# Optimization experiments

Hardware: AMD Instinct MI355X
Metric: run time of the kernel (lower is better)

## Reference

```python
import jax, jax.numpy as jnp
import numpy as np

B, C, H, W = 8, 512, 64, 128
K = 19          # num_classes
BH, BW = 2, 4   # bin_size
N = BH * BW     # bin_num
CI = C // 2     # feat_inner


def setup_inputs() -> dict:
    ks = jax.random.split(jax.random.key(0), 10)
    def nrm(k, shape, s=0.02):
        return jax.random.normal(k, shape, jnp.float32) * s
    return {
        "x": jax.random.normal(ks[0], (B, C, H, W), jnp.float32),
        "conv_cam_w": nrm(ks[1], (K, C)),
        "conv_cam_b": jnp.zeros((K,), jnp.float32),
        "gcn_w1": nrm(ks[2], (N, N), 0.1),
        "gcn_a": jnp.full((N,), 0.25, jnp.float32),
        "gcn_w2": nrm(ks[3], (C, C)),
        "fuse_w": nrm(ks[4], (1, N), 0.1),
        "fuse_b": jnp.zeros((1,), jnp.float32),
        "relu_a": jnp.full((1,), 0.25, jnp.float32),
        "q_w": nrm(ks[5], (CI, C)),
        "q_b": jnp.zeros((CI,), jnp.float32),
        "k_w": nrm(ks[6], (CI, C)),
        "k_b": jnp.zeros((CI,), jnp.float32),
        "v_w": nrm(ks[7], (CI, C)),
        "v_b": jnp.zeros((CI,), jnp.float32),
        "out_w": nrm(ks[8], (C, CI)),
        "bn_gamma": jnp.ones((C,), jnp.float32),
        "bn_beta": jnp.zeros((C,), jnp.float32),
        "out_a": jnp.full((C,), 0.25, jnp.float32),
    }


def _prelu(x, a):
    return jnp.maximum(x, 0) + a * jnp.minimum(x, 0)


def _split(t):
    # [b, cc, H, W] -> [b, N, rh*rw, cc]  (patch_split)
    b, cc = t.shape[0], t.shape[1]
    rh, rw = H // BH, W // BW
    t = t.reshape(b, cc, BH, rh, BW, rw).transpose(0, 2, 4, 3, 5, 1)
    return t.reshape(b, N, rh * rw, cc)


def _caam(x, conv_cam_w, conv_cam_b, gcn_w1, gcn_a, gcn_w2, fuse_w, fuse_b,
          relu_a, q_w, q_b, k_w, k_b, v_w, v_b, out_w, bn_gamma, bn_beta, out_a):
    b = x.shape[0]
    rh, rw = H // BH, W // BW
    # CAM (1x1 conv) + adaptive avg pool to bins + sigmoid
    cam = jnp.einsum('bchw,kc->bkhw', x, conv_cam_w) + conv_cam_b[None, :, None, None]
    cls_score = jax.nn.sigmoid(cam.reshape(b, K, BH, rh, BW, rw).mean((3, 5)))  # [b,K,BH,BW]
    cam_p = _split(cam)   # [b,N,P,K]
    x_p = _split(x)       # [b,N,P,C]
    bin_conf = cls_score.reshape(b, K, N).transpose(0, 2, 1)[..., None]  # [b,N,K,1]
    pix_conf = jax.nn.softmax(cam_p, axis=2)
    local = jnp.einsum('bnpk,bnpc->bnkc', pix_conf, x_p) * bin_conf  # [b,N,K,C]
    # GCN: conv1 over bin dim, PReLU(residual), Linear over channels
    t = jnp.einsum('nm,bmkc->bnkc', gcn_w1, local)
    t = _prelu(t + local, gcn_a[None, :, None, None])
    local = jnp.einsum('bnkc,dc->bnkd', t, gcn_w2)
    # fuse bins -> single global descriptor, PReLU(1)
    glob = jnp.einsum('on,bnkc->bokc', fuse_w, local) + fuse_b[None, :, None, None]  # [b,1,K,C]
    glob = _prelu(glob[:, 0], relu_a[0])  # [b,K,C]
    # QKV attention over bins (key/value over K class slots)
    q = jnp.einsum('bnpc,ic->bnpi', x_p, q_w) + q_b       # [b,N,P,CI]
    key = jnp.einsum('bnkc,ic->bnki', local, k_w) + k_b   # [b,N,K,CI]
    val = jnp.einsum('bkc,ic->bki', glob, v_w) + v_b      # [b,K,CI] (shared across bins)
    aff = jax.nn.softmax(jnp.einsum('bnpi,bnki->bnpk', q, key), axis=-1)
    out = jnp.einsum('bnpk,bki->bnpi', aff, val)          # [b,N,P,CI]
    # patch_recover -> [b,CI,H,W]
    out = out.reshape(b, BH, BW, rh, rw, CI).transpose(0, 5, 1, 3, 2, 4).reshape(b, CI, H, W)
    # conv_out: 1x1 conv (no bias) + BatchNorm2d (batch stats) + PReLU(C)
    y = jnp.einsum('bihw,ci->bchw', out, out_w)
    mu = y.mean((0, 2, 3), keepdims=True)
    var = y.var((0, 2, 3), keepdims=True)
    y = (y - mu) * jax.lax.rsqrt(var + 1e-5)
    y = y * bn_gamma[None, :, None, None] + bn_beta[None, :, None, None]
    y = _prelu(y, out_a[None, :, None, None])
    return x + y


def reference(x, conv_cam_w, conv_cam_b, gcn_w1, gcn_a, gcn_w2, fuse_w, fuse_b,
              relu_a, q_w, q_b, k_w, k_b, v_w, v_b, out_w, bn_gamma, bn_beta, out_a):
    return _caam(x, conv_cam_w, conv_cam_b, gcn_w1, gcn_a, gcn_w2, fuse_w, fuse_b,
                 relu_a, q_w, q_b, k_w, k_b, v_w, v_b, out_w, bn_gamma, bn_beta, out_a)
```

## Files before the change

### kernel.cpp

```cpp
#include <hip/hip_runtime.h>
#include <cstdint>
#include <cstddef>

#define B_ 8
#define C_ 512
#define H_ 64
#define W_ 128
#define HW_ 8192
#define K_ 19
#define N_ 8
#define P_ 1024
#define CI_ 256

typedef unsigned short u16;
typedef unsigned int u32;
typedef __attribute__((ext_vector_type(8))) short bf16x8;
typedef __attribute__((ext_vector_type(4))) float f32x4;

__device__ __forceinline__ u16 f2bf(float f) {
  u32 u = __float_as_uint(f);
  u32 r = (u + 0x7FFFu + ((u >> 16) & 1u)) >> 16;
  return (u16)r;
}
__device__ __forceinline__ float bf2f(u16 h) {
  return __uint_as_float(((u32)h) << 16);
}

__device__ __forceinline__ float blockSum256(float v, float* red4) {
#pragma unroll
  for (int o = 32; o > 0; o >>= 1) v += __shfl_down(v, o, 64);
  __syncthreads();
  if ((threadIdx.x & 63) == 0) red4[threadIdx.x >> 6] = v;
  __syncthreads();
  return red4[0] + red4[1] + red4[2] + red4[3];
}

__device__ __forceinline__ float blockMax256(float v, float* red4) {
#pragma unroll
  for (int o = 32; o > 0; o >>= 1) v = fmaxf(v, __shfl_down(v, o, 64));
  __syncthreads();
  if ((threadIdx.x & 63) == 0) red4[threadIdx.x >> 6] = v;
  __syncthreads();
  return fmaxf(fmaxf(red4[0], red4[1]), fmaxf(red4[2], red4[3]));
}

__global__ void zero_kernel(float* __restrict__ p) {
  p[blockIdx.x * 256 + threadIdx.x] = 0.f;
}

__global__ __launch_bounds__(256) void w2bf_kernel(const float* __restrict__ a,
                                                   u16* __restrict__ o) {
  int i = blockIdx.x * 256 + threadIdx.x;
  o[i] = f2bf(a[i]);
}

__global__ __launch_bounds__(256) void camw2bf_kernel(const float* __restrict__ a,
                                                      u16* __restrict__ o) {
  int i = blockIdx.x * 256 + threadIdx.x;
  o[i] = (i < K_ * C_) ? f2bf(a[i]) : (u16)0;
}

__global__ __launch_bounds__(256) void xpose_kernel(const float* __restrict__ x,
                                                    u16* __restrict__ xt) {
  __shared__ float tile[64][65];
  int bid = blockIdx.x;
  int hw0 = (bid & 127) << 6;
  int c0 = ((bid >> 7) & 7) << 6;
  int b = bid >> 10;
  int tid = threadIdx.x;
  int r = tid >> 4;
  int col4 = (tid & 15) << 2;
  const float* xb = x + ((size_t)b * C_ + c0) * HW_ + hw0;
#pragma unroll
  for (int it = 0; it < 4; it++) {
    int rr = r + it * 16;
    float4 v = *(const float4*)&xb[(size_t)rr * HW_ + col4];
    tile[rr][col4 + 0] = v.x;
    tile[rr][col4 + 1] = v.y;
    tile[rr][col4 + 2] = v.z;
    tile[rr][col4 + 3] = v.w;
  }
  __syncthreads();
  u16* xo = xt + ((size_t)b * HW_ + hw0) * C_ + c0;
#pragma unroll
  for (int it = 0; it < 4; it++) {
    int hwr = r + it * 16;
    ushort4 o;
    o.x = f2bf(tile[col4 + 0][hwr]);
    o.y = f2bf(tile[col4 + 1][hwr]);
    o.z = f2bf(tile[col4 + 2][hwr]);
    o.w = f2bf(tile[col4 + 3][hwr]);
    *(ushort4*)&xo[(size_t)hwr * C_ + col4] = o;
  }
}

__global__ __launch_bounds__(256) void gemm_cam_kernel(const u16* __restrict__ A,
                                                       const u16* __restrict__ Bw,
                                                       const float* __restrict__ bias,
                                                       float* __restrict__ cam) {
  __shared__ u16 As[128 * 72];
  __shared__ u16 Bs[32 * 72];
  int b = blockIdx.y;
  int m0 = blockIdx.x * 128;
  int tid = threadIdx.x;
  int wave = tid >> 6, lane = tid & 63;
  int wm = wave * 32;
  int quad = lane >> 4, l16 = lane & 15;
  const u16* Ab = A + (size_t)b * HW_ * C_ + (size_t)m0 * C_;
  f32x4 acc[2][2] = {};
  int sr = tid >> 3;
  int sk = (tid & 7) * 8;
  for (int k0 = 0; k0 < C_; k0 += 64) {
    __syncthreads();
#pragma unroll
    for (int it = 0; it < 4; it++) {
      int r = sr + it * 32;
      *(uint4*)&As[r * 72 + sk] = *(const uint4*)&Ab[(size_t)r * C_ + k0 + sk];
    }
    { int r = tid >> 3;
      *(uint4*)&Bs[r * 72 + sk] = *(const uint4*)&Bw[(size_t)r * C_ + k0 + sk]; }
    __syncthreads();
#pragma unroll
    for (int kk = 0; kk < 2; kk++) {
      bf16x8 af[2], bfv[2];
#pragma unroll
      for (int t = 0; t < 2; t++) {
        af[t] = *(const bf16x8*)&As[(wm + t * 16 + l16) * 72 + kk * 32 + quad * 8];
        bfv[t] = *(const bf16x8*)&Bs[(t * 16 + l16) * 72 + kk * 32 + quad * 8];
      }
#pragma unroll
      for (int tm = 0; tm < 2; tm++)
#pragma unroll
        for (int tn = 0; tn < 2; tn++)
          acc[tm][tn] = __builtin_amdgcn_mfma_f32_16x16x32_bf16(af[tm], bfv[tn], acc[tm][tn], 0, 0, 0);
    }
  }
  float* C = cam + (size_t)b * K_ * HW_;
#pragma unroll
  for (int tm = 0; tm < 2; tm++) {
    int mm = m0 + wm + tm * 16 + quad * 4;
#pragma unroll
    for (int tn = 0; tn < 2; tn++) {
      int nn = tn * 16 + l16;
      if (nn < K_) {
        float bv = bias[nn];
        f32x4 v = acc[tm][tn];
        v[0] += bv; v[1] += bv; v[2] += bv; v[3] += bv;
        *(f32x4*)&C[(size_t)nn * HW_ + mm] = v;
      }
    }
  }
}

__global__ __launch_bounds__(256) void softcls_kernel(const float* __restrict__ cam,
                                                      float* __restrict__ bconf,
                                                      float* __restrict__ pconf) {
  __shared__ float red4[4];
  int bid = blockIdx.x;
  int k = bid % 19;
  int n = (bid / 19) & 7;
  int b = bid / 152;
  int bh = n >> 2, bw = n & 3;
  const float* base = cam + ((size_t)b * K_ + k) * HW_ + (bh * 32) * W_ + bw * 32;
  float v[4];
  float s = 0.f, mx = -1e30f;
#pragma unroll
  for (int j = 0; j < 4; j++) {
    int p = threadIdx.x + j * 256;
    v[j] = base[(p >> 5) * W_ + (p & 31)];
    s += v[j];
    mx = fmaxf(mx, v[j]);
  }
  float tot = blockSum256(s, red4);
  if (threadIdx.x == 0) {
    float m = tot * (1.f / 1024.f);
    bconf[bid] = 1.f / (1.f + __expf(-m));
  }
  mx = blockMax256(mx, red4);
  float e[4];
  float se = 0.f;
#pragma unroll
  for (int j = 0; j < 4; j++) { e[j] = __expf(v[j] - mx); se += e[j]; }
  se = blockSum256(se, red4);
  float inv = 1.f / se;
  float* outp = pconf + (size_t)bid * P_;
#pragma unroll
  for (int j = 0; j < 4; j++) outp[threadIdx.x + j * 256] = e[j] * inv;
}

__global__ __launch_bounds__(256) void local_part_kernel(const u16* __restrict__ xt,
                                                         const float* __restrict__ pconf,
                                                         float* __restrict__ part) {
  __shared__ float pcl[19 * 256];
  int bid = blockIdx.x;
  int pq = bid & 3;
  int half = (bid >> 2) & 1;
  int n = (bid >> 3) & 7;
  int b = bid >> 6;
  int tid = threadIdx.x;
  int c = half * 256 + tid;
  int bh = n >> 2, bw = n & 3;
  const float* pcb = pconf + (size_t)((b * N_ + n) * K_) * P_ + pq * 256;
  for (int e = tid; e < 19 * 256; e += 256) {
    int k = e >> 8, pl = e & 255;
    pcl[e] = pcb[(size_t)k * P_ + pl];
  }
  __syncthreads();
  float acc[K_];
#pragma unroll
  for (int k = 0; k < K_; k++) acc[k] = 0.f;
  const u16* xb = xt + (size_t)b * HW_ * C_ + c;
#pragma unroll 4
  for (int pl = 0; pl < 256; pl++) {
    int p = pq * 256 + pl;
    int hw = (bh * 32 + (p >> 5)) * W_ + bw * 32 + (p & 31);
    float xv = bf2f(xb[(size_t)hw * C_]);
#pragma unroll
    for (int k = 0; k < K_; k++) acc[k] += pcl[k * 256 + pl] * xv;
  }
  int row = (b * N_ + n) * K_;
  float* pp = part + ((size_t)pq * 1216 + row) * C_ + c;
#pragma unroll
  for (int k = 0; k < K_; k++) pp[(size_t)k * C_] = acc[k];
}

__global__ __launch_bounds__(256) void local_reduce_kernel(const float* __restrict__ part,
                                                           const float* __restrict__ bconf,
                                                           float* __restrict__ locl) {
  int idx = blockIdx.x * 256 + threadIdx.x;
  int r = idx >> 9;
  float s = part[idx] + part[idx + 1216 * 512] + part[idx + 2 * 1216 * 512] + part[idx + 3 * 1216 * 512];
  locl[idx] = s * bconf[r];
}

__global__ __launch_bounds__(256) void t_kernel(const float* __restrict__ locl,
                                                const float* __restrict__ gw1,
                                                const float* __restrict__ ga,
                                                u16* __restrict__ tbuf) {
  __shared__ float gw1l[64];
  __shared__ float gal[8];
  int tid = threadIdx.x;
  if (tid < 64) gw1l[tid] = gw1[tid];
  if (tid < 8) gal[tid] = ga[tid];
  __syncthreads();
  int bid = blockIdx.x;
  int half = bid & 1;
  int rem = bid >> 1;
  int k = rem % 19;
  int b = rem / 19;
  int c = half * 256 + tid;
  const float* lb = locl + ((size_t)(b * N_) * K_ + k) * C_ + c;
  float lm[8];
#pragma unroll
  for (int m = 0; m < 8; m++) lm[m] = lb[(size_t)m * K_ * C_];
#pragma unroll
  for (int n = 0; n < 8; n++) {
    float v = lm[n];
#pragma unroll
    for (int m = 0; m < 8; m++) v += gw1l[n * 8 + m] * lm[m];
    float t = fmaxf(v, 0.f) + gal[n] * fminf(v, 0.f);
    tbuf[((size_t)((b * N_ + n) * K_ + k)) * C_ + c] = f2bf(t);
  }
}

template <int KDIM, int NDIM, bool BIAS>
__global__ __launch_bounds__(256) void gemm_small_kernel(const u16* __restrict__ A,
                                                         const u16* __restrict__ Bw,
                                                         const float* __restrict__ bias,
                                                         float* __restrict__ f32out,
                                                         u16* __restrict__ bf16out) {
  __shared__ u16 As[128 * 72];
  __shared__ u16 Bs[128 * 72];
  constexpr int NT = NDIM / 128;
  int m0 = (blockIdx.x / NT) * 128;
  int n0 = (blockIdx.x % NT) * 128;
  int tid = threadIdx.x;
  int wave = tid >> 6, lane = tid & 63;
  int wm = (wave >> 1) * 64, wn = (wave & 1) * 64;
  int quad = lane >> 4, l16 = lane & 15;
  const u16* Ab = A + (size_t)m0 * KDIM;
  const u16* Bb = Bw + (size_t)n0 * KDIM;
  f32x4 acc[4][4] = {};
  int sr = tid >> 3;
  int sk = (tid & 7) * 8;
  for (int k0 = 0; k0 < KDIM; k0 += 64) {
    __syncthreads();
#pragma unroll
    for (int it = 0; it < 4; it++) {
      int r = sr + it * 32;
      *(uint4*)&As[r * 72 + sk] = *(const uint4*)&Ab[(size_t)r * KDIM + k0 + sk];
      *(uint4*)&Bs[r * 72 + sk] = *(const uint4*)&Bb[(size_t)r * KDIM + k0 + sk];
    }
    __syncthreads();
#pragma unroll
    for (int kk = 0; kk < 2; kk++) {
      bf16x8 af[4], bfv[4];
#pragma unroll
      for (int t = 0; t < 4; t++) {
        af[t] = *(const bf16x8*)&As[(wm + t * 16 + l16) * 72 + kk * 32 + quad * 8];
        bfv[t] = *(const bf16x8*)&Bs[(wn + t * 16 + l16) * 72 + kk * 32 + quad * 8];
      }
#pragma unroll
      for (int tm = 0; tm < 4; tm++)
#pragma unroll
        for (int tn = 0; tn < 4; tn++)
          acc[tm][tn] = __builtin_amdgcn_mfma_f32_16x16x32_bf16(af[tm], bfv[tn], acc[tm][tn], 0, 0, 0);
    }
  }
  float bv[4];
#pragma unroll
  for (int tn = 0; tn < 4; tn++)
    bv[tn] = BIAS ? bias[n0 + wn + tn * 16 + l16] : 0.f;
#pragma unroll
  for (int tm = 0; tm < 4; tm++) {
    int mm = m0 + wm + tm * 16 + quad * 4;
#pragma unroll
    for (int tn = 0; tn < 4; tn++) {
      int nn = n0 + wn + tn * 16 + l16;
#pragma unroll
      for (int reg = 0; reg < 4; reg++) {
        float v = acc[tm][tn][reg] + bv[tn];
        if (f32out) f32out[(size_t)(mm + reg) * NDIM + nn] = v;
        if (bf16out) bf16out[(size_t)(mm + reg) * NDIM + nn] = f2bf(v);
      }
    }
  }
}

__global__ __launch_bounds__(256) void glob_val_kernel(const float* __restrict__ locl2,
                                                       const float* __restrict__ fw,
                                                       const float* __restrict__ fb,
                                                       const float* __restrict__ ra,
                                                       const float* __restrict__ vw,
                                                       const float* __restrict__ vb,
                                                       float* __restrict__ valo) {
  __shared__ __align__(16) float gl[512];
  int bid = blockIdx.x;
  int k = bid % 19;
  int b = bid / 19;
  int tid = threadIdx.x;
  float fwr[8];
#pragma unroll
  for (int m = 0; m < 8; m++) fwr[m] = fw[m];
  float fbv = fb[0], rav = ra[0];
  const float* lb = locl2 + ((size_t)(b * N_) * K_ + k) * C_;
  for (int c = tid; c < C_; c += 256) {
    float v = fbv;
#pragma unroll
    for (int m = 0; m < 8; m++) v += fwr[m] * lb[(size_t)m * K_ * C_ + c];
    gl[c] = fmaxf(v, 0.f) + rav * fminf(v, 0.f);
  }
  __syncthreads();
  int i = tid;
  const float* wr = vw + (size_t)i * C_;
  float s = vb[i];
  for (int c4 = 0; c4 < C_; c4 += 4) {
    float4 wv = *(const float4*)&wr[c4];
    float4 tv = *(const float4*)&gl[c4];
    s += wv.x * tv.x + wv.y * tv.y + wv.z * tv.z + wv.w * tv.w;
  }
  valo[(size_t)bid * CI_ + i] = s;
}

template <int KDIM, int NDIM, bool TRANS_OUT, bool BIAS, bool OUTBF16, bool BNSTAT>
__global__ __launch_bounds__(256) void gemm_big_kernel(const u16* __restrict__ A,
                                                       const u16* __restrict__ Bw,
                                                       const float* __restrict__ bias,
                                                       void* __restrict__ Cout,
                                                       float* __restrict__ sums,
                                                       float* __restrict__ sumsq) {
  __shared__ u16 As[128 * 72];
  __shared__ u16 Bs[128 * 72];
  constexpr int NT = NDIM / 128;
  int b = blockIdx.y;
  int m0 = (blockIdx.x / NT) * 128;
  int n0 = (blockIdx.x % NT) * 128;
  int tid = threadIdx.x;
  int wave = tid >> 6, lane = tid & 63;
  int wm = (wave >> 1) * 64, wn = (wave & 1) * 64;
  int quad = lane >> 4, l16 = lane & 15;
  const u16* Ab = A + (size_t)b * 8192 * KDIM + (size_t)m0 * KDIM;
  const u16* Bb = Bw + (size_t)n0 * KDIM;
  f32x4 acc[4][4] = {};
  int sr = tid >> 3;
  int sk = (tid & 7) * 8;
  for (int k0 = 0; k0 < KDIM; k0 += 64) {
    __syncthreads();
#pragma unroll
    for (int it = 0; it < 4; it++) {
      int r = sr + it * 32;
      *(uint4*)&As[r * 72 + sk] = *(const uint4*)&Ab[(size_t)r * KDIM + k0 + sk];
      *(uint4*)&Bs[r * 72 + sk] = *(const uint4*)&Bb[(size_t)r * KDIM + k0 + sk];
    }
    __syncthreads();
#pragma unroll
    for (int kk = 0; kk < 2; kk++) {
      bf16x8 af[4], bfv[4];
#pragma unroll
      for (int t = 0; t < 4; t++) {
        af[t] = *(const bf16x8*)&As[(wm + t * 16 + l16) * 72 + kk * 32 + quad * 8];
        bfv[t] = *(const bf16x8*)&Bs[(wn + t * 16 + l16) * 72 + kk * 32 + quad * 8];
      }
#pragma unroll
      for (int tm = 0; tm < 4; tm++)
#pragma unroll
        for (int tn = 0; tn < 4; tn++)
          acc[tm][tn] = __builtin_amdgcn_mfma_f32_16x16x32_bf16(af[tm], bfv[tn], acc[tm][tn], 0, 0, 0);
    }
  }
  if constexpr (!TRANS_OUT) {
    float bv[4];
#pragma unroll
    for (int tn = 0; tn < 4; tn++)
      bv[tn] = BIAS ? bias[n0 + wn + tn * 16 + l16] : 0.f;
#pragma unroll
    for (int tm = 0; tm < 4; tm++) {
      int mm = m0 + wm + tm * 16 + quad * 4;
#pragma unroll
      for (int tn = 0; tn < 4; tn++) {
        int nn = n0 + wn + tn * 16 + l16;
        if constexpr (OUTBF16) {
          u16* C = (u16*)Cout + (size_t)b * 8192 * NDIM;
#pragma unroll
          for (int reg = 0; reg < 4; reg++)
            C[(size_t)(mm + reg) * NDIM + nn] = f2bf(acc[tm][tn][reg] + bv[tn]);
        } else {
          float* C = (float*)Cout + (size_t)b * 8192 * NDIM;
#pragma unroll
          for (int reg = 0; reg < 4; reg++)
            C[(size_t)(mm + reg) * NDIM + nn] = acc[tm][tn][reg] + bv[tn];
        }
      }
    }
  } else {
    float* C = (float*)Cout + (size_t)b * NDIM * 8192;
#pragma unroll
    for (int tm = 0; tm < 4; tm++) {
      int mm = m0 + wm + tm * 16 + quad * 4;
#pragma unroll
      for (int tn = 0; tn < 4; tn++) {
        int nn = n0 + wn + tn * 16 + l16;
        *(f32x4*)&C[(size_t)nn * 8192 + mm] = acc[tm][tn];
      }
    }
    if constexpr (BNSTAT) {
#pragma unroll
      for (int tn = 0; tn < 4; tn++) {
        int nn = n0 + wn + tn * 16 + l16;
        float s = 0.f, q = 0.f;
#pragma unroll
        for (int tm = 0; tm < 4; tm++)
#pragma unroll
          for (int reg = 0; reg < 4; reg++) {
            float v = acc[tm][tn][reg];
            s += v;
            q += v * v;
          }
        s += __shfl_xor(s, 16, 64); q += __shfl_xor(q, 16, 64);
        s += __shfl_xor(s, 32, 64); q += __shfl_xor(q, 32, 64);
        if (quad == 0) {
          atomicAdd(&sums[nn], s);
          atomicAdd(&sumsq[nn], q);
        }
      }
    }
  }
}

__global__ __launch_bounds__(256) void attn2_kernel(const u16* __restrict__ q,
                                                    const float* __restrict__ keyo,
                                                    const float* __restrict__ valo,
                                                    u16* __restrict__ obuf) {
  __shared__ float keyl[19 * 256];
  __shared__ float vall[19 * 256];
  __shared__ float aff[128 * 20];
  int bid = blockIdx.x;
  int rg = bid & 7;
  int n = (bid >> 3) & 7;
  int b = bid >> 6;
  int bh = n >> 2, bw = n & 3;
  int tid = threadIdx.x;
  const float* ksrc = keyo + (size_t)((b * 8 + n) * 19) * 256;
  for (int e = tid; e < 19 * 256; e += 256) keyl[e] = ksrc[e];
  __syncthreads();
  if (tid < 128) {
    int r = rg * 4 + (tid >> 5);
    int wc = tid & 31;
    int hw = (bh * 32 + r) * W_ + bw * 32 + wc;
    const u16* qr = q + ((size_t)b * HW_ + hw) * 256;
    float acc[19];
#pragma unroll
    for (int k = 0; k < 19; k++) acc[k] = 0.f;
    for (int i0 = 0; i0 < 256; i0 += 8) {
      uint4 v = *(const uint4*)&qr[i0];
      float f0 = __uint_as_float((v.x & 0xFFFFu) << 16);
      float f1 = __uint_as_float(v.x & 0xFFFF0000u);
      float f2 = __uint_as_float((v.y & 0xFFFFu) << 16);
      float f3 = __uint_as_float(v.y & 0xFFFF0000u);
      float f4 = __uint_as_float((v.z & 0xFFFFu) << 16);
      float f5 = __uint_as_float(v.z & 0xFFFF0000u);
      float f6 = __uint_as_float((v.w & 0xFFFFu) << 16);
      float f7 = __uint_as_float(v.w & 0xFFFF0000u);
#pragma unroll
      for (int k = 0; k < 19; k++) {
        const float* kr = &keyl[k * 256 + i0];
        acc[k] += f0 * kr[0] + f1 * kr[1] + f2 * kr[2] + f3 * kr[3] +
                  f4 * kr[4] + f5 * kr[5] + f6 * kr[6] + f7 * kr[7];
      }
    }
    float mx = -1e30f;
#pragma unroll
    for (int k = 0; k < 19; k++) mx = fmaxf(mx, acc[k]);
    float se = 0.f;
#pragma unroll
    for (int k = 0; k < 19; k++) { acc[k] = __expf(acc[k] - mx); se += acc[k]; }
    float inv = 1.f / se;
#pragma unroll
    for (int k = 0; k < 19; k++) aff[tid * 20 + k] = acc[k] * inv;
  } else {
    const float* vsrc = valo + (size_t)b * 19 * 256;
    for (int e = tid - 128; e < 19 * 256; e += 128) vall[e] = vsrc[e];
  }
  __syncthreads();
  int px = tid & 127;
  int ih = (tid >> 7) * 128;
  int r3 = rg * 4 + (px >> 5);
  int wc3 = px & 31;
  int hw3 = (bh * 32 + r3) * W_ + bw * 32 + wc3;
  float av[19];
#pragma unroll
  for (int k = 0; k < 19; k++) av[k] = aff[px * 20 + k];
  u16* ob = obuf + ((size_t)b * HW_ + hw3) * 256 + ih;
  for (int i0 = 0; i0 < 128; i0 += 16) {
    float o16[16];
#pragma unroll
    for (int j = 0; j < 16; j++) o16[j] = 0.f;
#pragma unroll
    for (int k = 0; k < 19; k++) {
      float a = av[k];
      const float* vr = &vall[k * 256 + ih + i0];
#pragma unroll
      for (int j = 0; j < 16; j++) o16[j] += a * vr[j];
    }
    uint4 w0, w1;
    w0.x = (u32)f2bf(o16[0]) | ((u32)f2bf(o16[1]) << 16);
    w0.y = (u32)f2bf(o16[2]) | ((u32)f2bf(o16[3]) << 16);
    w0.z = (u32)f2bf(o16[4]) | ((u32)f2bf(o16[5]) << 16);
    w0.w = (u32)f2bf(o16[6]) | ((u32)f2bf(o16[7]) << 16);
    w1.x = (u32)f2bf(o16[8]) | ((u32)f2bf(o16[9]) << 16);
    w1.y = (u32)f2bf(o16[10]) | ((u32)f2bf(o16[11]) << 16);
    w1.z = (u32)f2bf(o16[12]) | ((u32)f2bf(o16[13]) << 16);
    w1.w = (u32)f2bf(o16[14]) | ((u32)f2bf(o16[15]) << 16);
    *(uint4*)&ob[i0] = w0;
    *(uint4*)&ob[i0 + 8] = w1;
  }
}

__global__ __launch_bounds__(512) void bnfinal_kernel(const float* __restrict__ sums,
                                                      const float* __restrict__ sumsq,
                                                      const float* __restrict__ gamma,
                                                      const float* __restrict__ beta,
                                                      float* __restrict__ scale,
                                                      float* __restrict__ shift) {
  int c = threadIdx.x;
  const float inv_cnt = 1.f / 65536.f;
  float mu = sums[c] * inv_cnt;
  float var = sumsq[c] * inv_cnt - mu * mu;
  float iv = rsqrtf(var + 1e-5f);
  float sc = gamma[c] * iv;
  scale[c] = sc;
  shift[c] = beta[c] - mu * sc;
}

__global__ __launch_bounds__(256) void final_kernel(const float* __restrict__ x,
                                                    const float* __restrict__ scale,
                                                    const float* __restrict__ shift,
                                                    const float* __restrict__ oa,
                                                    float* __restrict__ out) {
  size_t idx = ((size_t)blockIdx.x * 256 + threadIdx.x) * 4;
  int c = (int)((idx >> 13) & 511);
  float sc = scale[c], sh = shift[c], a = oa[c];
  float4 y = *(float4*)&out[idx];
  float4 xv = *(const float4*)&x[idx];
  float4 r;
  float t;
  t = y.x * sc + sh; r.x = xv.x + fmaxf(t, 0.f) + a * fminf(t, 0.f);
  t = y.y * sc + sh; r.y = xv.y + fmaxf(t, 0.f) + a * fminf(t, 0.f);
  t = y.z * sc + sh; r.z = xv.z + fmaxf(t, 0.f) + a * fminf(t, 0.f);
  t = y.w * sc + sh; r.w = xv.w + fmaxf(t, 0.f) + a * fminf(t, 0.f);
  *(float4*)&out[idx] = r;
}

extern "C" void kernel_launch(void* const* d_in, const int* in_sizes, int n_in,
                              void* d_out, int out_size, void* d_ws, size_t ws_size,
                              hipStream_t stream) {
  const float* x     = (const float*)d_in[0];
  const float* camw  = (const float*)d_in[1];
  const float* camb  = (const float*)d_in[2];
  const float* gw1   = (const float*)d_in[3];
  const float* ga    = (const float*)d_in[4];
  const float* gw2   = (const float*)d_in[5];
  const float* fw    = (const float*)d_in[6];
  const float* fb    = (const float*)d_in[7];
  const float* ra    = (const float*)d_in[8];
  const float* qw    = (const float*)d_in[9];
  const float* qb    = (const float*)d_in[10];
  const float* kw    = (const float*)d_in[11];
  const float* kb    = (const float*)d_in[12];
  const float* vw    = (const float*)d_in[13];
  const float* vb    = (const float*)d_in[14];
  const float* ow    = (const float*)d_in[15];
  const float* gamma = (const float*)d_in[16];
  const float* beta  = (const float*)d_in[17];
  const float* oa    = (const float*)d_in[18];
  float* out = (float*)d_out;
  float* ws = (float*)d_ws;

  float* cam    = ws;
  float* bconf  = cam + 1245184;
  float* pconf  = bconf + 2048;
  float* locl   = pconf + 1245184;
  float* locl2f = locl + 622592;
  float* keyo   = locl2f + 655360;
  float* valo   = keyo + 327680;
  float* sums   = valo + 38912;
  float* sumsq  = sums + 512;
  float* scale  = sumsq + 512;
  float* shift  = scale + 512;
  u16* qwbf   = (u16*)(shift + 512);
  u16* owbf   = qwbf + 131072;
  u16* kwbf   = owbf + 131072;
  u16* gw2bf  = kwbf + 131072;
  u16* camwbf = gw2bf + 262144;
  u16* tbuf   = camwbf + 16384;
  u16* l2bf   = tbuf + 655360;
  u16* xt     = l2bf + 655360;
  u16* obuf   = xt;
  u16* qbuf   = xt + 33554432;
  float* part = (float*)qbuf;

  zero_kernel<<<4, 256, 0, stream>>>(sums);
  w2bf_kernel<<<512, 256, 0, stream>>>(qw, qwbf);
  w2bf_kernel<<<512, 256, 0, stream>>>(ow, owbf);
  w2bf_kernel<<<512, 256, 0, stream>>>(kw, kwbf);
  w2bf_kernel<<<1024, 256, 0, stream>>>(gw2, gw2bf);
  camw2bf_kernel<<<64, 256, 0, stream>>>(camw, camwbf);
  zero_kernel<<<64, 256, 0, stream>>>((float*)(tbuf + 1216 * 512));

  xpose_kernel<<<8192, 256, 0, stream>>>(x, xt);
  gemm_cam_kernel<<<dim3(64, 8), 256, 0, stream>>>(xt, camwbf, camb, cam);
  softcls_kernel<<<1216, 256, 0, stream>>>(cam, bconf, pconf);
  local_part_kernel<<<512, 256, 0, stream>>>(xt, pconf, part);
  local_reduce_kernel<<<2432, 256, 0, stream>>>(part, bconf, locl);
  t_kernel<<<304, 256, 0, stream>>>(locl, gw1, ga, tbuf);
  gemm_small_kernel<512, 512, false>
      <<<40, 256, 0, stream>>>(tbuf, gw2bf, nullptr, locl2f, l2bf);
  gemm_small_kernel<512, 256, true>
      <<<20, 256, 0, stream>>>(l2bf, kwbf, kb, keyo, nullptr);
  glob_val_kernel<<<152, 256, 0, stream>>>(locl2f, fw, fb, ra, vw, vb, valo);
  gemm_big_kernel<512, 256, false, true, true, false>
      <<<dim3(128, 8), 256, 0, stream>>>(xt, qwbf, qb, qbuf, nullptr, nullptr);
  attn2_kernel<<<512, 256, 0, stream>>>(qbuf, keyo, valo, obuf);
  gemm_big_kernel<256, 512, true, false, false, true>
      <<<dim3(256, 8), 256, 0, stream>>>(obuf, owbf, nullptr, out, sums, sumsq);
  bnfinal_kernel<<<1, 512, 0, stream>>>(sums, sumsq, gamma, beta, scale, shift);
  final_kernel<<<32768, 256, 0, stream>>>(x, scale, shift, oa, out);
}
```

Measured before the change: 578.2 us.

## Merge prep kernels, fuse local reduce into t_kernel, vectorize loads, XCD-aware tile mapping

Folds the six weight-conversion and zeroing launches into one vectorized prep kernel, and folds the partial-sum reduction and bin-confidence scaling into t_kernel, which removes a launch and a round trip through the locl buffer. local_part_kernel now loads pconf with float4 and batches eight pixel loads per step with vectorized shared-memory reads. gemm_big remaps block indices so consecutive blocks on the same XCD share an M tile. final_kernel processes four float4 per thread with fewer blocks. These cut launch overhead and memory traffic, at the cost of more index arithmetic and a different L2 access pattern.

```diff
diff --git a/kernel.cpp b/kernel.cpp
--- a/kernel.cpp
+++ b/kernel.cpp
@@ -44,20 +44,50 @@
   return fmaxf(fmaxf(red4[0], red4[1]), fmaxf(red4[2], red4[3]));
 }
 
-__global__ void zero_kernel(float* __restrict__ p) {
-  p[blockIdx.x * 256 + threadIdx.x] = 0.f;
-}
-
-__global__ __launch_bounds__(256) void w2bf_kernel(const float* __restrict__ a,
-                                                   u16* __restrict__ o) {
-  int i = blockIdx.x * 256 + threadIdx.x;
-  o[i] = f2bf(a[i]);
-}
-
-__global__ __launch_bounds__(256) void camw2bf_kernel(const float* __restrict__ a,
-                                                      u16* __restrict__ o) {
-  int i = blockIdx.x * 256 + threadIdx.x;
-  o[i] = (i < K_ * C_) ? f2bf(a[i]) : (u16)0;
+__device__ __forceinline__ void cvt4(const float* __restrict__ s, u16* __restrict__ d, int i) {
+  float4 v = *(const float4*)&s[(size_t)i * 4];
+  ushort4 o;
+  o.x = f2bf(v.x); o.y = f2bf(v.y); o.z = f2bf(v.z); o.w = f2bf(v.w);
+  *(ushort4*)&d[(size_t)i * 4] = o;
+}
+
+__global__ __launch_bounds__(256) void prep_kernel(const float* __restrict__ qw,
+                                                   const float* __restrict__ ow,
+                                                   const float* __restrict__ kw,
+                                                   const float* __restrict__ gw2,
+                                                   const float* __restrict__ camw,
+                                                   u16* __restrict__ qwbf,
+                                                   u16* __restrict__ owbf,
+                                                   u16* __restrict__ kwbf,
+                                                   u16* __restrict__ gw2bf,
+                                                   u16* __restrict__ camwbf,
+                                                   float* __restrict__ sums,
+                                                   float* __restrict__ tpad) {
+  int bid = blockIdx.x, tid = threadIdx.x;
+  if (bid < 128) {
+    cvt4(qw, qwbf, bid * 256 + tid);
+  } else if (bid < 256) {
+    cvt4(ow, owbf, (bid - 128) * 256 + tid);
+  } else if (bid < 384) {
+    cvt4(kw, kwbf, (bid - 256) * 256 + tid);
+  } else if (bid < 640) {
+    cvt4(gw2, gw2bf, (bid - 384) * 256 + tid);
+  } else if (bid < 656) {
+    int i = (bid - 640) * 256 + tid;
+    if (i * 4 < K_ * C_) {
+      cvt4(camw, camwbf, i);
+    } else {
+      ushort4 z; z.x = 0; z.y = 0; z.z = 0; z.w = 0;
+      *(ushort4*)&camwbf[(size_t)i * 4] = z;
+    }
+  } else if (bid == 656) {
+    float4 z; z.x = 0.f; z.y = 0.f; z.z = 0.f; z.w = 0.f;
+    *(float4*)&sums[tid * 4] = z;
+  } else {
+    int i = (bid - 657) * 256 + tid;
+    float4 z; z.x = 0.f; z.y = 0.f; z.z = 0.f; z.w = 0.f;
+    *(float4*)&tpad[(size_t)i * 4] = z;
+  }
 }
 
 __global__ __launch_bounds__(256) void xpose_kernel(const float* __restrict__ x,
@@ -191,7 +221,7 @@
 __global__ __launch_bounds__(256) void local_part_kernel(const u16* __restrict__ xt,
                                                          const float* __restrict__ pconf,
                                                          float* __restrict__ part) {
-  __shared__ float pcl[19 * 256];
+  __shared__ __align__(16) float pcl[19 * 256];
   int bid = blockIdx.x;
   int pq = bid & 3;
   int half = (bid >> 2) & 1;
@@ -201,22 +231,32 @@
   int c = half * 256 + tid;
   int bh = n >> 2, bw = n & 3;
   const float* pcb = pconf + (size_t)((b * N_ + n) * K_) * P_ + pq * 256;
-  for (int e = tid; e < 19 * 256; e += 256) {
-    int k = e >> 8, pl = e & 255;
-    pcl[e] = pcb[(size_t)k * P_ + pl];
+  for (int e = tid; e < 19 * 64; e += 256) {
+    int k = e >> 6, q4 = e & 63;
+    *(float4*)&pcl[k * 256 + q4 * 4] = *(const float4*)&pcb[(size_t)k * P_ + q4 * 4];
   }
   __syncthreads();
   float acc[K_];
 #pragma unroll
   for (int k = 0; k < K_; k++) acc[k] = 0.f;
   const u16* xb = xt + (size_t)b * HW_ * C_ + c;
-#pragma unroll 4
-  for (int pl = 0; pl < 256; pl++) {
-    int p = pq * 256 + pl;
-    int hw = (bh * 32 + (p >> 5)) * W_ + bw * 32 + (p & 31);
-    float xv = bf2f(xb[(size_t)hw * C_]);
-#pragma unroll
-    for (int k = 0; k < K_; k++) acc[k] += pcl[k * 256 + pl] * xv;
+  for (int pl0 = 0; pl0 < 256; pl0 += 8) {
+    float xv[8];
+#pragma unroll
+    for (int g = 0; g < 2; g++) {
+      int p = pq * 256 + pl0 + g * 4;
+      int hw = (bh * 32 + (p >> 5)) * W_ + bw * 32 + (p & 31);
+      const u16* xr = xb + (size_t)hw * C_;
+#pragma unroll
+      for (int j = 0; j < 4; j++) xv[g * 4 + j] = bf2f(xr[(size_t)j * C_]);
+    }
+#pragma unroll
+    for (int k = 0; k < K_; k++) {
+      float4 p0 = *(const float4*)&pcl[k * 256 + pl0];
+      float4 p1 = *(const float4*)&pcl[k * 256 + pl0 + 4];
+      acc[k] += p0.x * xv[0] + p0.y * xv[1] + p0.z * xv[2] + p0.w * xv[3]
+              + p1.x * xv[4] + p1.y * xv[5] + p1.z * xv[6] + p1.w * xv[7];
+    }
   }
   int row = (b * N_ + n) * K_;
   float* pp = part + ((size_t)pq * 1216 + row) * C_ + c;
@@ -224,35 +264,34 @@
   for (int k = 0; k < K_; k++) pp[(size_t)k * C_] = acc[k];
 }
 
-__global__ __launch_bounds__(256) void local_reduce_kernel(const float* __restrict__ part,
-                                                           const float* __restrict__ bconf,
-                                                           float* __restrict__ locl) {
-  int idx = blockIdx.x * 256 + threadIdx.x;
-  int r = idx >> 9;
-  float s = part[idx] + part[idx + 1216 * 512] + part[idx + 2 * 1216 * 512] + part[idx + 3 * 1216 * 512];
-  locl[idx] = s * bconf[r];
-}
-
-__global__ __launch_bounds__(256) void t_kernel(const float* __restrict__ locl,
+__global__ __launch_bounds__(256) void t_kernel(const float* __restrict__ part,
+                                                const float* __restrict__ bconf,
                                                 const float* __restrict__ gw1,
                                                 const float* __restrict__ ga,
                                                 u16* __restrict__ tbuf) {
   __shared__ float gw1l[64];
   __shared__ float gal[8];
+  __shared__ float bcl[8];
   int tid = threadIdx.x;
-  if (tid < 64) gw1l[tid] = gw1[tid];
-  if (tid < 8) gal[tid] = ga[tid];
-  __syncthreads();
   int bid = blockIdx.x;
   int half = bid & 1;
   int rem = bid >> 1;
   int k = rem % 19;
   int b = rem / 19;
+  if (tid < 64) gw1l[tid] = gw1[tid];
+  if (tid < 8) {
+    gal[tid] = ga[tid];
+    bcl[tid] = bconf[(size_t)(b * 8 + tid) * 19 + k];
+  }
+  __syncthreads();
   int c = half * 256 + tid;
-  const float* lb = locl + ((size_t)(b * N_) * K_ + k) * C_ + c;
   float lm[8];
 #pragma unroll
-  for (int m = 0; m < 8; m++) lm[m] = lb[(size_t)m * K_ * C_];
+  for (int m = 0; m < 8; m++) {
+    size_t off = ((size_t)(b * N_ + m) * K_ + k) * C_ + c;
+    lm[m] = (part[off] + part[off + (size_t)1216 * 512] +
+             part[off + (size_t)2 * 1216 * 512] + part[off + (size_t)3 * 1216 * 512]) * bcl[m];
+  }
 #pragma unroll
   for (int n = 0; n < 8; n++) {
     float v = lm[n];
@@ -373,8 +412,11 @@
   __shared__ u16 Bs[128 * 72];
   constexpr int NT = NDIM / 128;
   int b = blockIdx.y;
-  int m0 = (blockIdx.x / NT) * 128;
-  int n0 = (blockIdx.x % NT) * 128;
+  int d = blockIdx.x;
+  int xcd = d & 7;
+  int j = d >> 3;
+  int m0 = (xcd + 8 * (j / NT)) * 128;
+  int n0 = (j % NT) * 128;
   int tid = threadIdx.x;
   int wave = tid >> 6, lane = tid & 63;
   int wm = (wave >> 1) * 64, wn = (wave & 1) * 64;
@@ -577,18 +619,22 @@
                                                     const float* __restrict__ shift,
                                                     const float* __restrict__ oa,
                                                     float* __restrict__ out) {
-  size_t idx = ((size_t)blockIdx.x * 256 + threadIdx.x) * 4;
-  int c = (int)((idx >> 13) & 511);
+  size_t base = (size_t)blockIdx.x * 4096 + threadIdx.x * 4;
+  int c = (int)((base >> 13) & 511);
   float sc = scale[c], sh = shift[c], a = oa[c];
-  float4 y = *(float4*)&out[idx];
-  float4 xv = *(const float4*)&x[idx];
-  float4 r;
-  float t;
-  t = y.x * sc + sh; r.x = xv.x + fmaxf(t, 0.f) + a * fminf(t, 0.f);
-  t = y.y * sc + sh; r.y = xv.y + fmaxf(t, 0.f) + a * fminf(t, 0.f);
-  t = y.z * sc + sh; r.z = xv.z + fmaxf(t, 0.f) + a * fminf(t, 0.f);
-  t = y.w * sc + sh; r.w = xv.w + fmaxf(t, 0.f) + a * fminf(t, 0.f);
-  *(float4*)&out[idx] = r;
+#pragma unroll
+  for (int jj = 0; jj < 4; jj++) {
+    size_t idx = base + (size_t)jj * 1024;
+    float4 y = *(float4*)&out[idx];
+    float4 xv = *(const float4*)&x[idx];
+    float4 r;
+    float t;
+    t = y.x * sc + sh; r.x = xv.x + fmaxf(t, 0.f) + a * fminf(t, 0.f);
+    t = y.y * sc + sh; r.y = xv.y + fmaxf(t, 0.f) + a * fminf(t, 0.f);
+    t = y.z * sc + sh; r.z = xv.z + fmaxf(t, 0.f) + a * fminf(t, 0.f);
+    t = y.w * sc + sh; r.w = xv.w + fmaxf(t, 0.f) + a * fminf(t, 0.f);
+    *(float4*)&out[idx] = r;
+  }
 }
 
 extern "C" void kernel_launch(void* const* d_in, const int* in_sizes, int n_in,
@@ -639,20 +685,14 @@
   u16* qbuf   = xt + 33554432;
   float* part = (float*)qbuf;
 
-  zero_kernel<<<4, 256, 0, stream>>>(sums);
-  w2bf_kernel<<<512, 256, 0, stream>>>(qw, qwbf);
-  w2bf_kernel<<<512, 256, 0, stream>>>(ow, owbf);
-  w2bf_kernel<<<512, 256, 0, stream>>>(kw, kwbf);
-  w2bf_kernel<<<1024, 256, 0, stream>>>(gw2, gw2bf);
-  camw2bf_kernel<<<64, 256, 0, stream>>>(camw, camwbf);
-  zero_kernel<<<64, 256, 0, stream>>>((float*)(tbuf + 1216 * 512));
-
+  prep_kernel<<<673, 256, 0, stream>>>(qw, ow, kw, gw2, camw,
+                                       qwbf, owbf, kwbf, gw2bf, camwbf,
+                                       sums, (float*)(tbuf + 1216 * 512));
   xpose_kernel<<<8192, 256, 0, stream>>>(x, xt);
   gemm_cam_kernel<<<dim3(64, 8), 256, 0, stream>>>(xt, camwbf, camb, cam);
   softcls_kernel<<<1216, 256, 0, stream>>>(cam, bconf, pconf);
   local_part_kernel<<<512, 256, 0, stream>>>(xt, pconf, part);
-  local_reduce_kernel<<<2432, 256, 0, stream>>>(part, bconf, locl);
-  t_kernel<<<304, 256, 0, stream>>>(locl, gw1, ga, tbuf);
+  t_kernel<<<304, 256, 0, stream>>>(part, bconf, gw1, ga, tbuf);
   gemm_small_kernel<512, 512, false>
       <<<40, 256, 0, stream>>>(tbuf, gw2bf, nullptr, locl2f, l2bf);
   gemm_small_kernel<512, 256, true>
@@ -664,5 +704,5 @@
   gemm_big_kernel<256, 512, true, false, false, true>
       <<<dim3(256, 8), 256, 0, stream>>>(obuf, owbf, nullptr, out, sums, sumsq);
   bnfinal_kernel<<<1, 512, 0, stream>>>(sums, sumsq, gamma, beta, scale, shift);
-  final_kernel<<<32768, 256, 0, stream>>>(x, scale, shift, oa, out);
-}
+  final_kernel<<<8192, 256, 0, stream>>>(x, scale, shift, oa, out);
+}
```

Measured after the change: 569.2 us. No clear change (-1.6%).
